# Kernel optimization log

Measured on AMD Instinct MI355X. Metric: run time of the kernel, lower is better.

## Reference

```python
import jax, jax.numpy as jnp
import numpy as np

N = 100000      # num_nodes
E = 1200000     # num_edges (avg degree 12)
F_IN = 64       # num_features
H = 64          # args.hidden_dim
C = 40          # num_classes


def setup_inputs() -> dict:
    key = jax.random.key(0)
    ks = jax.random.split(key, 8)
    x = jax.random.normal(ks[0], (N, F_IN), jnp.float32)
    edge_index = jax.random.randint(ks[1], (2, E), 0, N, dtype=jnp.int64)
    edge_attr = jax.random.uniform(ks[2], (E,), jnp.float32)

    def glorot(k, fi, fo):
        return jax.random.normal(k, (fi, fo), jnp.float32) * jnp.sqrt(2.0 / (fi + fo))

    return {
        "x": x, "edge_index": edge_index, "edge_attr": edge_attr,
        "W1": glorot(ks[3], F_IN, H), "b1": jnp.zeros((H,), jnp.float32),
        "W2": glorot(ks[4], H, H),    "b2": jnp.zeros((H,), jnp.float32),
        "W3": glorot(ks[5], H, H),    "b3": jnp.zeros((H,), jnp.float32),
        "W4": glorot(ks[6], H, C),    "b4": jnp.zeros((C,), jnp.float32),
    }


def _gcn_layer(h, W, b, src, dst, norm):
    # GCNConv: linear transform, gather source features, weight by symmetric
    # norm, scatter-add at targets, add bias.
    h = h @ W                                   # [N, out]
    msg = h[src] * norm[:, None]                # [E+N, out]
    out = jax.ops.segment_sum(msg, dst, num_segments=N)
    return out + b


def reference(x, edge_index, edge_attr, W1, b1, W2, b2, W3, b3, W4, b4):
    # Add self-loops with weight 1 (PyG GCNConv default fill_value=1.)
    loop = jnp.arange(N, dtype=edge_index.dtype)
    src = jnp.concatenate([edge_index[0], loop])
    dst = jnp.concatenate([edge_index[1], loop])
    w = jnp.concatenate([edge_attr, jnp.ones((N,), edge_attr.dtype)])
    # Symmetric normalization: deg^{-1/2}[src] * w * deg^{-1/2}[dst]
    deg = jax.ops.segment_sum(w, dst, num_segments=N)
    dis = jnp.where(deg > 0, jax.lax.rsqrt(jnp.maximum(deg, 1e-12)), 0.0)
    norm = dis[src] * w * dis[dst]

    h = jax.nn.elu(_gcn_layer(x, W1, b1, src, dst, norm))
    h = jax.nn.elu(_gcn_layer(h, W2, b2, src, dst, norm))
    h = jax.nn.elu(_gcn_layer(h, W3, b3, src, dst, norm))
    h = _gcn_layer(h, W4, b4, src, dst, norm)
    return jax.nn.log_softmax(h, axis=1)
```

## Files before the change

### kernel.cpp

```cpp
#include <hip/hip_runtime.h>
#include <hip/hip_fp16.h>
#include <cstdint>
#include <cmath>


#define NPB_SHIFT 9
#define NPB 512
#define CHUNK 4096

__device__ __forceinline__ float fdot2f(__half2 a, __half2 b, float c) {
#if defined(__has_builtin)
#if __has_builtin(__builtin_amdgcn_fdot2)
    typedef _Float16 h2v __attribute__((ext_vector_type(2)));
    return __builtin_amdgcn_fdot2(__builtin_bit_cast(h2v, a),
                                  __builtin_bit_cast(h2v, b), c, false);
#else
    float2 fa = __half22float2(a), fb = __half22float2(b);
    return fmaf(fa.x, fb.x, fmaf(fa.y, fb.y, c));
#endif
#else
    float2 fa = __half22float2(a), fb = __half22float2(b);
    return fmaf(fa.x, fb.x, fmaf(fa.y, fb.y, c));
#endif
}

__device__ __forceinline__ void wave_lds_fence() {
    asm volatile("s_waitcnt lgkmcnt(0)" ::: "memory");
    __builtin_amdgcn_wave_barrier();
    __builtin_amdgcn_sched_barrier(0);
}


__global__ __launch_bounds__(256) void bucket_init_kernel(int* __restrict__ bucket_cnt,
                                                          int nbuck) {
    if ((int)threadIdx.x < nbuck) bucket_cnt[threadIdx.x] = 0;
}

__global__ __launch_bounds__(256) void bucket_count_kernel(const int* __restrict__ dst,
                                                           int* __restrict__ bucket_cnt,
                                                           int* __restrict__ blockbase,
                                                           int nbuck, int E) {
    __shared__ int hist[256];
    int tid = threadIdx.x;
    hist[tid] = 0;
    __syncthreads();
    int base = blockIdx.x * CHUNK;
    #pragma unroll
    for (int u = 0; u < CHUNK / 256; ++u) {
        int e = base + u * 256 + tid;
        if (e < E) atomicAdd(&hist[dst[e] >> NPB_SHIFT], 1);
    }
    __syncthreads();
    if (tid < nbuck)
        blockbase[blockIdx.x * nbuck + tid] = atomicAdd(&bucket_cnt[tid], hist[tid]);
}

__global__ __launch_bounds__(64) void bucket_scan_kernel(const int* __restrict__ bucket_cnt,
                                                         int* __restrict__ bucket_base,
                                                         int nbuck, int E) {
    int lane = threadIdx.x;
    int run = 0;
    for (int b0 = 0; b0 < nbuck; b0 += 64) {
        int i = b0 + lane;
        int v = (i < nbuck) ? bucket_cnt[i] : 0;
        int x = v;
        #pragma unroll
        for (int off = 1; off < 64; off <<= 1) {
            int t = __shfl_up(x, off);
            if (lane >= off) x += t;
        }
        if (i < nbuck) bucket_base[i] = run + x - v;
        run += __shfl(x, 63);
    }
    if (lane == 0) bucket_base[nbuck] = E;
}

__global__ __launch_bounds__(256) void bucket_scatter_kernel(const int* __restrict__ src,
                                                             const int* __restrict__ dst,
                                                             const float* __restrict__ w,
                                                             const int* __restrict__ bucket_base,
                                                             const int* __restrict__ blockbase,
                                                             int2* __restrict__ temp,
                                                             int nbuck, int E) {
    __shared__ int cursor[256];
    int tid = threadIdx.x;
    if (tid < nbuck)
        cursor[tid] = bucket_base[tid] + blockbase[blockIdx.x * nbuck + tid];
    __syncthreads();
    int base = blockIdx.x * CHUNK;
    #pragma unroll
    for (int u = 0; u < CHUNK / 256; ++u) {
        int e = base + u * 256 + tid;
        if (e < E) {
            int d = dst[e];
            int pos = atomicAdd(&cursor[d >> NPB_SHIFT], 1);
            temp[pos] = make_int2(src[e] | ((d & (NPB - 1)) << 17),
                                  __float_as_int(w[e]));
        }
    }
}

__global__ __launch_bounds__(256) void bucket_csr_kernel(const int2* __restrict__ temp,
                                                         const int* __restrict__ bucket_base,
                                                         int* __restrict__ offsets,
                                                         int2* __restrict__ pairs,
                                                         int n, int E) {
    __shared__ int cnt[NPB];
    __shared__ int wtot[4];
    int tid = threadIdx.x;
    int bk = blockIdx.x;
    int base = bucket_base[bk], end = bucket_base[bk + 1];
    cnt[tid] = 0; cnt[tid + 256] = 0;
    __syncthreads();
    for (int j = base + tid; j < end; j += 256)
        atomicAdd(&cnt[temp[j].x >> 17], 1);
    __syncthreads();
    int a0 = cnt[2 * tid], a1 = cnt[2 * tid + 1];
    int s = a0 + a1;
    int lane = tid & 63, wid = tid >> 6;
    int x = s;
    #pragma unroll
    for (int off = 1; off < 64; off <<= 1) {
        int t2 = __shfl_up(x, off);
        if (lane >= off) x += t2;
    }
    if (lane == 63) wtot[wid] = x;
    __syncthreads();
    int wbase = 0;
    #pragma unroll
    for (int wv = 0; wv < 4; ++wv) if (wv < wid) wbase += wtot[wv];
    int e0 = wbase + x - s;
    int abs0 = base + e0, abs1 = base + e0 + a0;
    int node0 = bk * NPB + 2 * tid;
    if (node0 < n)     offsets[node0]     = abs0;
    if (node0 + 1 < n) offsets[node0 + 1] = abs1;
    __syncthreads();
    cnt[2 * tid] = abs0; cnt[2 * tid + 1] = abs1;
    __syncthreads();
    for (int j = base + tid; j < end; j += 256) {
        int2 t2 = temp[j];
        int pos = atomicAdd(&cnt[t2.x >> 17], 1);
        pairs[pos] = make_int2(t2.x & 0x1FFFF, t2.y);
    }
    if (bk == 0 && tid == 0) offsets[n] = E;
}

__global__ __launch_bounds__(256) void rowsum_scale_kernel(const int* __restrict__ offsets,
                                                           const int2* __restrict__ pairs,
                                                           const float* __restrict__ x,
                                                           float* __restrict__ dis,
                                                           __half* __restrict__ g, int n) {
    int node = blockIdx.x * 16 + (threadIdx.x >> 4);
    int q = threadIdx.x & 15;
    if (node >= n) return;
    int j0 = offsets[node], end = offsets[node + 1];
    float s = 0.f;
    for (int j = j0 + q; j < end; j += 16) s += __int_as_float(pairs[j].y);
    #pragma unroll
    for (int off = 8; off; off >>= 1) s += __shfl_xor(s, off);
    float dn = rsqrtf(1.0f + s);
    if (q == 0) dis[node] = dn;
    float4 v = reinterpret_cast<const float4*>(x)[(size_t)node * 16 + q];
    __half2 pk[2];
    pk[0] = __float22half2_rn(make_float2(dn * v.x, dn * v.y));
    pk[1] = __float22half2_rn(make_float2(dn * v.z, dn * v.w));
    reinterpret_cast<float2*>(g + (size_t)node * 64)[q] = *reinterpret_cast<float2*>(pk);
}

__device__ __forceinline__ void accum8(float* acc, float4 rv, float w) {
    const __half2* h = reinterpret_cast<const __half2*>(&rv);
    #pragma unroll
    for (int k = 0; k < 4; ++k) {
        float2 f = __half22float2(h[k]);
        acc[2 * k]     = fmaf(w, f.x, acc[2 * k]);
        acc[2 * k + 1] = fmaf(w, f.y, acc[2 * k + 1]);
    }
}

__device__ __forceinline__ void agg_node(const float4* __restrict__ gt,
                                         const int2* __restrict__ pairs,
                                         int j, int end, int node, int q,
                                         float* __restrict__ acc) {
    for (; j + 4 <= end; j += 4) {
        int2 p0 = pairs[j], p1 = pairs[j + 1], p2 = pairs[j + 2], p3 = pairs[j + 3];
        float4 r0 = gt[(size_t)p0.x * 8 + q];
        float4 r1 = gt[(size_t)p1.x * 8 + q];
        float4 r2 = gt[(size_t)p2.x * 8 + q];
        float4 r3 = gt[(size_t)p3.x * 8 + q];
        accum8(acc, r0, __int_as_float(p0.y));
        accum8(acc, r1, __int_as_float(p1.y));
        accum8(acc, r2, __int_as_float(p2.y));
        accum8(acc, r3, __int_as_float(p3.y));
    }
    for (; j < end; ++j) {
        int2 p = pairs[j];
        float4 r = gt[(size_t)p.x * 8 + q];
        accum8(acc, r, __int_as_float(p.y));
    }
    float4 rs = gt[(size_t)node * 8 + q];
    accum8(acc, rs, 1.0f);
}

__device__ __forceinline__ void phase1_agg(const __half* __restrict__ gin,
                                           const float* __restrict__ dis,
                                           const int* __restrict__ offsets,
                                           const int2* __restrict__ pairs,
                                           __half2 (*rows)[33], int n, int tid,
                                           int blockbase_node) {
    int ln = tid >> 3;
    int q  = tid & 7;
    int gnode = blockbase_node + ln;
    if (gnode < n) {
        const float4* gt = reinterpret_cast<const float4*>(gin);
        float acc[8] = {0.f, 0.f, 0.f, 0.f, 0.f, 0.f, 0.f, 0.f};
        agg_node(gt, pairs, offsets[gnode], offsets[gnode + 1], gnode, q, acc);
        float dn = dis[gnode];
        #pragma unroll
        for (int k2 = 0; k2 < 4; ++k2)
            rows[ln][q * 4 + k2] =
                __float22half2_rn(make_float2(dn * acc[2 * k2], dn * acc[2 * k2 + 1]));
    }
}

__global__ __launch_bounds__(256) void layer_fused_kernel(const __half* __restrict__ gin,
                                                          const float* __restrict__ dis,
                                                          const int* __restrict__ offsets,
                                                          const int2* __restrict__ pairs,
                                                          const float* __restrict__ W,
                                                          const float* __restrict__ b,
                                                          __half* __restrict__ gout, int n) {
    __shared__ __half2 rows[32][33];
    __shared__ __half2 WT[64][33];
    __shared__ float bias_s[64];
    for (int idx = threadIdx.x; idx < 64 * 32; idx += 256) {
        int k2 = idx >> 6, c = idx & 63;
        WT[c][k2] = __float22half2_rn(make_float2(W[(2 * k2) * 64 + c],
                                                  W[(2 * k2 + 1) * 64 + c]));
    }
    if (threadIdx.x < 64) bias_s[threadIdx.x] = b[threadIdx.x];
    __syncthreads();

    int tid = threadIdx.x;
    phase1_agg(gin, dis, offsets, pairs, rows, n, tid, blockIdx.x * 32);
    wave_lds_fence();

    int lane  = tid & 63, wave = tid >> 6;
    int node2 = wave * 8 + (lane & 7);
    int slice = lane >> 3;
    int gnode2 = blockIdx.x * 32 + node2;
    if (gnode2 < n) {
        __half2 h2[32];
        #pragma unroll
        for (int i = 0; i < 32; ++i) h2[i] = rows[node2][i];
        float dn = dis[gnode2];
        int c0 = slice * 8;
        float r[8];
        #pragma unroll
        for (int cc = 0; cc < 8; ++cc) {
            const __half2* wt = &WT[c0 + cc][0];
            float a0 = 0.f, a1 = 0.f, a2 = 0.f, a3 = 0.f;
            #pragma unroll
            for (int i = 0; i < 8; ++i) {
                a0 = fdot2f(h2[4 * i],     wt[4 * i],     a0);
                a1 = fdot2f(h2[4 * i + 1], wt[4 * i + 1], a1);
                a2 = fdot2f(h2[4 * i + 2], wt[4 * i + 2], a2);
                a3 = fdot2f(h2[4 * i + 3], wt[4 * i + 3], a3);
            }
            float v = (a0 + a1) + (a2 + a3) + bias_s[c0 + cc];
            v = (v > 0.f) ? v : expm1f(v);
            r[cc] = dn * v;
        }
        __half2 pk[4];
        pk[0] = __float22half2_rn(make_float2(r[0], r[1]));
        pk[1] = __float22half2_rn(make_float2(r[2], r[3]));
        pk[2] = __float22half2_rn(make_float2(r[4], r[5]));
        pk[3] = __float22half2_rn(make_float2(r[6], r[7]));
        *reinterpret_cast<float4*>(gout + (size_t)gnode2 * 64 + c0) =
            *reinterpret_cast<float4*>(pk);
    }
}

__global__ __launch_bounds__(256) void layer4_fused_kernel(const __half* __restrict__ gin,
                                                           const float* __restrict__ dis,
                                                           const int* __restrict__ offsets,
                                                           const int2* __restrict__ pairs,
                                                           const float* __restrict__ W,
                                                           const float* __restrict__ b,
                                                           float* __restrict__ out, int n) {
    __shared__ __half2 rows[32][33];
    __shared__ __half2 WT[40][33];
    __shared__ float bias_s[40];
    for (int idx = threadIdx.x; idx < 40 * 32; idx += 256) {
        int c = idx % 40, k2 = idx / 40;
        WT[c][k2] = __float22half2_rn(make_float2(W[(2 * k2) * 40 + c],
                                                  W[(2 * k2 + 1) * 40 + c]));
    }
    if (threadIdx.x < 40) bias_s[threadIdx.x] = b[threadIdx.x];
    __syncthreads();

    int tid = threadIdx.x;
    phase1_agg(gin, dis, offsets, pairs, rows, n, tid, blockIdx.x * 32);
    wave_lds_fence();

    int lane  = tid & 63, wave = tid >> 6;
    int node2 = wave * 8 + (lane & 7);
    int slice = lane >> 3;
    int gnode2 = blockIdx.x * 32 + node2;

    float r[5];
    float mp = -__builtin_inff();
    if (gnode2 < n) {
        __half2 h2[32];
        #pragma unroll
        for (int i = 0; i < 32; ++i) h2[i] = rows[node2][i];
        int c0 = slice * 5;
        #pragma unroll
        for (int cc = 0; cc < 5; ++cc) {
            const __half2* wt = &WT[c0 + cc][0];
            float a0 = 0.f, a1 = 0.f, a2 = 0.f, a3 = 0.f;
            #pragma unroll
            for (int i = 0; i < 8; ++i) {
                a0 = fdot2f(h2[4 * i],     wt[4 * i],     a0);
                a1 = fdot2f(h2[4 * i + 1], wt[4 * i + 1], a1);
                a2 = fdot2f(h2[4 * i + 2], wt[4 * i + 2], a2);
                a3 = fdot2f(h2[4 * i + 3], wt[4 * i + 3], a3);
            }
            r[cc] = (a0 + a1) + (a2 + a3) + bias_s[c0 + cc];
            mp = fmaxf(mp, r[cc]);
        }
    }
    mp = fmaxf(mp, __shfl_xor(mp, 8));
    mp = fmaxf(mp, __shfl_xor(mp, 16));
    mp = fmaxf(mp, __shfl_xor(mp, 32));
    float sp = 0.f;
    if (gnode2 < n) {
        #pragma unroll
        for (int cc = 0; cc < 5; ++cc) sp += expf(r[cc] - mp);
    }
    sp += __shfl_xor(sp, 8);
    sp += __shfl_xor(sp, 16);
    sp += __shfl_xor(sp, 32);
    if (gnode2 < n) {
        float ls = logf(sp) + mp;
        float* outp = out + (size_t)gnode2 * 40 + slice * 5;
        #pragma unroll
        for (int cc = 0; cc < 5; ++cc) outp[cc] = r[cc] - ls;
    }
}


static inline size_t align_up(size_t x, size_t a) { return (x + a - 1) & ~(a - 1); }

extern "C" void kernel_launch(void* const* d_in, const int* in_sizes, int n_in,
                              void* d_out, int out_size, void* d_ws, size_t ws_size,
                              hipStream_t stream) {
    const float* x  = (const float*)d_in[0];
    const int*   ei = (const int*)d_in[1];
    const float* ea = (const float*)d_in[2];
    const float* W1 = (const float*)d_in[3];
    const float* b1 = (const float*)d_in[4];
    const float* W2 = (const float*)d_in[5];
    const float* b2 = (const float*)d_in[6];
    const float* W3 = (const float*)d_in[7];
    const float* b3 = (const float*)d_in[8];
    const float* W4 = (const float*)d_in[9];
    const float* b4 = (const float*)d_in[10];

    const int N = in_sizes[0] / 64;
    const int E = in_sizes[1] / 2;

    const int* src = ei;
    const int* dst = ei + E;

    const int nbuck   = (N + NPB - 1) >> NPB_SHIFT;
    const int nblk_ac = (E + CHUNK - 1) / CHUNK;

    char* p = (char*)d_ws;
    int*    offsets     = (int*)p;  p += align_up(((size_t)N + 1) * 4, 256);
    int*    bucket_cnt  = (int*)p;  p += align_up(((size_t)nbuck + 1) * 4, 256);
    int*    bucket_base = (int*)p;  p += align_up(((size_t)nbuck + 1) * 4, 256);
    int*    blockbase   = (int*)p;  p += align_up((size_t)nblk_ac * nbuck * 4, 256);
    float*  dis         = (float*)p; p += align_up((size_t)N * 4, 256);
    int2*   pairs       = (int2*)p;  p += align_up(((size_t)E + 8) * 8, 256);
    int2*   temp        = (int2*)p;  p += align_up(((size_t)E + 8) * 8, 256);
    __half* gA          = (__half*)p; p += align_up((size_t)N * 64 * 2, 256);
    __half* gB          = (__half*)p; p += align_up((size_t)N * 64 * 2, 256);
    (void)ws_size;

    const int nb_g16 = (N + 15) / 16;
    const int nb_f   = (N + 31) / 32;

    bucket_init_kernel<<<1, 256, 0, stream>>>(bucket_cnt, nbuck);
    bucket_count_kernel<<<nblk_ac, 256, 0, stream>>>(dst, bucket_cnt, blockbase, nbuck, E);
    bucket_scan_kernel<<<1, 64, 0, stream>>>(bucket_cnt, bucket_base, nbuck, E);
    bucket_scatter_kernel<<<nblk_ac, 256, 0, stream>>>(src, dst, ea, bucket_base,
                                                       blockbase, temp, nbuck, E);
    bucket_csr_kernel<<<nbuck, 256, 0, stream>>>(temp, bucket_base, offsets, pairs, N, E);
    rowsum_scale_kernel<<<nb_g16, 256, 0, stream>>>(offsets, pairs, x, dis, gA, N);

    layer_fused_kernel<<<nb_f, 256, 0, stream>>>(gA, dis, offsets, pairs, W1, b1, gB, N);
    layer_fused_kernel<<<nb_f, 256, 0, stream>>>(gB, dis, offsets, pairs, W2, b2, gA, N);
    layer_fused_kernel<<<nb_f, 256, 0, stream>>>(gA, dis, offsets, pairs, W3, b3, gB, N);

    layer4_fused_kernel<<<nb_f, 256, 0, stream>>>(gB, dis, offsets, pairs, W4, b4,
                                                  (float*)d_out, N);
}
```

Measured before the change: 207.7 us.

## Accumulate aggregation in packed fp16, unroll gathers by eight, remap lane-to-node

Edge weights are stored as half2 in the CSR pairs, and neighbour aggregation accumulates with packed fp16 FMA (__hfma2) instead of unpacking to fp32. This halves the accumulator registers and the per-edge ALU work. The gather loop is unrolled to 8 independent loads to raise memory-level parallelism. The transform phase also remaps lanes so consecutive lanes share a node, which turns the softmax shuffles into short xor distances. The cost is reduced accumulation precision, since fp16 sums over about 13 terms risk rounding error or overflow.

```diff
diff --git a/kernel.cpp b/kernel.cpp
--- a/kernel.cpp
+++ b/kernel.cpp
@@ -140,7 +140,8 @@
     for (int j = base + tid; j < end; j += 256) {
         int2 t2 = temp[j];
         int pos = atomicAdd(&cnt[t2.x >> 17], 1);
-        pairs[pos] = make_int2(t2.x & 0x1FFFF, t2.y);
+        __half2 w2 = __float2half2_rn(__int_as_float(t2.y));
+        pairs[pos] = make_int2(t2.x & 0x1FFFF, *reinterpret_cast<int*>(&w2));
     }
     if (bk == 0 && tid == 0) offsets[n] = E;
 }
@@ -155,7 +156,10 @@
     if (node >= n) return;
     int j0 = offsets[node], end = offsets[node + 1];
     float s = 0.f;
-    for (int j = j0 + q; j < end; j += 16) s += __int_as_float(pairs[j].y);
+    for (int j = j0 + q; j < end; j += 16) {
+        int wb = pairs[j].y;
+        s += __low2float(*reinterpret_cast<__half2*>(&wb));
+    }
     #pragma unroll
     for (int off = 8; off; off >>= 1) s += __shfl_xor(s, off);
     float dn = rsqrtf(1.0f + s);
@@ -167,38 +171,46 @@
     reinterpret_cast<float2*>(g + (size_t)node * 64)[q] = *reinterpret_cast<float2*>(pk);
 }
 
-__device__ __forceinline__ void accum8(float* acc, float4 rv, float w) {
+__device__ __forceinline__ void accum_pk(__half2* acc, float4 rv, int wbits) {
+    __half2 w2 = *reinterpret_cast<__half2*>(&wbits);
     const __half2* h = reinterpret_cast<const __half2*>(&rv);
-    #pragma unroll
-    for (int k = 0; k < 4; ++k) {
-        float2 f = __half22float2(h[k]);
-        acc[2 * k]     = fmaf(w, f.x, acc[2 * k]);
-        acc[2 * k + 1] = fmaf(w, f.y, acc[2 * k + 1]);
-    }
+    acc[0] = __hfma2(w2, h[0], acc[0]);
+    acc[1] = __hfma2(w2, h[1], acc[1]);
+    acc[2] = __hfma2(w2, h[2], acc[2]);
+    acc[3] = __hfma2(w2, h[3], acc[3]);
 }
 
 __device__ __forceinline__ void agg_node(const float4* __restrict__ gt,
                                          const int2* __restrict__ pairs,
                                          int j, int end, int node, int q,
-                                         float* __restrict__ acc) {
-    for (; j + 4 <= end; j += 4) {
-        int2 p0 = pairs[j], p1 = pairs[j + 1], p2 = pairs[j + 2], p3 = pairs[j + 3];
+                                         __half2* __restrict__ acc) {
+    for (; j + 8 <= end; j += 8) {
+        int2 p[8];
+        #pragma unroll
+        for (int u = 0; u < 8; ++u) p[u] = pairs[j + u];
+        float4 r[8];
+        #pragma unroll
+        for (int u = 0; u < 8; ++u) r[u] = gt[(size_t)p[u].x * 8 + q];
+        #pragma unroll
+        for (int u = 0; u < 8; ++u) accum_pk(acc, r[u], p[u].y);
+    }
+    for (; j + 2 <= end; j += 2) {
+        int2 p0 = pairs[j], p1 = pairs[j + 1];
         float4 r0 = gt[(size_t)p0.x * 8 + q];
         float4 r1 = gt[(size_t)p1.x * 8 + q];
-        float4 r2 = gt[(size_t)p2.x * 8 + q];
-        float4 r3 = gt[(size_t)p3.x * 8 + q];
-        accum8(acc, r0, __int_as_float(p0.y));
-        accum8(acc, r1, __int_as_float(p1.y));
-        accum8(acc, r2, __int_as_float(p2.y));
-        accum8(acc, r3, __int_as_float(p3.y));
-    }
-    for (; j < end; ++j) {
+        accum_pk(acc, r0, p0.y);
+        accum_pk(acc, r1, p1.y);
+    }
+    if (j < end) {
         int2 p = pairs[j];
-        float4 r = gt[(size_t)p.x * 8 + q];
-        accum8(acc, r, __int_as_float(p.y));
+        accum_pk(acc, gt[(size_t)p.x * 8 + q], p.y);
     }
     float4 rs = gt[(size_t)node * 8 + q];
-    accum8(acc, rs, 1.0f);
+    const __half2* h = reinterpret_cast<const __half2*>(&rs);
+    acc[0] = __hadd2(acc[0], h[0]);
+    acc[1] = __hadd2(acc[1], h[1]);
+    acc[2] = __hadd2(acc[2], h[2]);
+    acc[3] = __hadd2(acc[3], h[3]);
 }
 
 __device__ __forceinline__ void phase1_agg(const __half* __restrict__ gin,
@@ -212,13 +224,15 @@
     int gnode = blockbase_node + ln;
     if (gnode < n) {
         const float4* gt = reinterpret_cast<const float4*>(gin);
-        float acc[8] = {0.f, 0.f, 0.f, 0.f, 0.f, 0.f, 0.f, 0.f};
+        __half2 acc[4];
+        acc[0] = acc[1] = acc[2] = acc[3] = __float2half2_rn(0.f);
         agg_node(gt, pairs, offsets[gnode], offsets[gnode + 1], gnode, q, acc);
         float dn = dis[gnode];
         #pragma unroll
-        for (int k2 = 0; k2 < 4; ++k2)
-            rows[ln][q * 4 + k2] =
-                __float22half2_rn(make_float2(dn * acc[2 * k2], dn * acc[2 * k2 + 1]));
+        for (int k2 = 0; k2 < 4; ++k2) {
+            float2 f = __half22float2(acc[k2]);
+            rows[ln][q * 4 + k2] = __float22half2_rn(make_float2(dn * f.x, dn * f.y));
+        }
     }
 }
 
@@ -245,8 +259,8 @@
     wave_lds_fence();
 
     int lane  = tid & 63, wave = tid >> 6;
-    int node2 = wave * 8 + (lane & 7);
-    int slice = lane >> 3;
+    int node2 = wave * 8 + (lane >> 3);
+    int slice = lane & 7;
     int gnode2 = blockIdx.x * 32 + node2;
     if (gnode2 < n) {
         __half2 h2[32];
@@ -303,8 +317,8 @@
     wave_lds_fence();
 
     int lane  = tid & 63, wave = tid >> 6;
-    int node2 = wave * 8 + (lane & 7);
-    int slice = lane >> 3;
+    int node2 = wave * 8 + (lane >> 3);
+    int slice = lane & 7;
     int gnode2 = blockIdx.x * 32 + node2;
 
     float r[5];
@@ -329,17 +343,17 @@
             mp = fmaxf(mp, r[cc]);
         }
     }
-    mp = fmaxf(mp, __shfl_xor(mp, 8));
-    mp = fmaxf(mp, __shfl_xor(mp, 16));
-    mp = fmaxf(mp, __shfl_xor(mp, 32));
+    mp = fmaxf(mp, __shfl_xor(mp, 1));
+    mp = fmaxf(mp, __shfl_xor(mp, 2));
+    mp = fmaxf(mp, __shfl_xor(mp, 4));
     float sp = 0.f;
     if (gnode2 < n) {
         #pragma unroll
         for (int cc = 0; cc < 5; ++cc) sp += expf(r[cc] - mp);
     }
-    sp += __shfl_xor(sp, 8);
-    sp += __shfl_xor(sp, 16);
-    sp += __shfl_xor(sp, 32);
+    sp += __shfl_xor(sp, 1);
+    sp += __shfl_xor(sp, 2);
+    sp += __shfl_xor(sp, 4);
     if (gnode2 < n) {
         float ls = logf(sp) + mp;
         float* outp = out + (size_t)gnode2 * 40 + slice * 5;
```

Result: slower. 218.2 us (+5.1%).

## Process two nodes per thread group in fused layers with interleaved gathers

Applied to the files above, without the earlier changes.

The fused GCN layer kernel now handles 64 nodes per block, and each 8-thread group aggregates two nodes with an interleaved loop that issues four independent row gathers at a time. The aim is more memory-level parallelism per thread and half as many blocks, each loading the transposed weights once. The transform phase runs two passes over the LDS rows. The bucket counter init kernel is also replaced by hipMemsetAsync. The risks are extra register pressure and imbalance when the two nodes have very different degrees.

```diff
diff --git a/kernel.cpp b/kernel.cpp
--- a/kernel.cpp
+++ b/kernel.cpp
@@ -31,11 +31,6 @@
 }
 
 
-__global__ __launch_bounds__(256) void bucket_init_kernel(int* __restrict__ bucket_cnt,
-                                                          int nbuck) {
-    if ((int)threadIdx.x < nbuck) bucket_cnt[threadIdx.x] = 0;
-}
-
 __global__ __launch_bounds__(256) void bucket_count_kernel(const int* __restrict__ dst,
                                                            int* __restrict__ bucket_cnt,
                                                            int* __restrict__ blockbase,
@@ -177,9 +172,9 @@
     }
 }
 
-__device__ __forceinline__ void agg_node(const float4* __restrict__ gt,
+__device__ __forceinline__ void agg_tail(const float4* __restrict__ gt,
                                          const int2* __restrict__ pairs,
-                                         int j, int end, int node, int q,
+                                         int j, int end, int q,
                                          float* __restrict__ acc) {
     for (; j + 4 <= end; j += 4) {
         int2 p0 = pairs[j], p1 = pairs[j + 1], p2 = pairs[j + 2], p3 = pairs[j + 3];
@@ -197,8 +192,121 @@
         float4 r = gt[(size_t)p.x * 8 + q];
         accum8(acc, r, __int_as_float(p.y));
     }
-    float4 rs = gt[(size_t)node * 8 + q];
-    accum8(acc, rs, 1.0f);
+}
+
+__device__ __forceinline__ void phase1_agg_dual(const __half* __restrict__ gin,
+                                                const float* __restrict__ dis,
+                                                const int* __restrict__ offsets,
+                                                const int2* __restrict__ pairs,
+                                                __half2 (*rows)[33], int n, int tid,
+                                                int base_node) {
+    int g = tid >> 3;
+    int q = tid & 7;
+    int nA = base_node + g;
+    int nB = base_node + 32 + g;
+    const float4* gt = reinterpret_cast<const float4*>(gin);
+
+    float accA[8] = {0.f, 0.f, 0.f, 0.f, 0.f, 0.f, 0.f, 0.f};
+    float accB[8] = {0.f, 0.f, 0.f, 0.f, 0.f, 0.f, 0.f, 0.f};
+    int jA = 0, eA = 0, jB = 0, eB = 0;
+    if (nA < n) { jA = offsets[nA]; eA = offsets[nA + 1]; }
+    if (nB < n) { jB = offsets[nB]; eB = offsets[nB + 1]; }
+
+    while (jA + 2 <= eA && jB + 2 <= eB) {
+        int2 a0 = pairs[jA], a1 = pairs[jA + 1];
+        int2 b0 = pairs[jB], b1 = pairs[jB + 1];
+        float4 rA0 = gt[(size_t)a0.x * 8 + q];
+        float4 rA1 = gt[(size_t)a1.x * 8 + q];
+        float4 rB0 = gt[(size_t)b0.x * 8 + q];
+        float4 rB1 = gt[(size_t)b1.x * 8 + q];
+        accum8(accA, rA0, __int_as_float(a0.y));
+        accum8(accA, rA1, __int_as_float(a1.y));
+        accum8(accB, rB0, __int_as_float(b0.y));
+        accum8(accB, rB1, __int_as_float(b1.y));
+        jA += 2; jB += 2;
+    }
+    agg_tail(gt, pairs, jA, eA, q, accA);
+    agg_tail(gt, pairs, jB, eB, q, accB);
+
+    if (nA < n) {
+        float4 rs = gt[(size_t)nA * 8 + q];
+        accum8(accA, rs, 1.0f);
+        float dn = dis[nA];
+        #pragma unroll
+        for (int k2 = 0; k2 < 4; ++k2)
+            rows[g][q * 4 + k2] =
+                __float22half2_rn(make_float2(dn * accA[2 * k2], dn * accA[2 * k2 + 1]));
+    }
+    if (nB < n) {
+        float4 rs = gt[(size_t)nB * 8 + q];
+        accum8(accB, rs, 1.0f);
+        float dn = dis[nB];
+        #pragma unroll
+        for (int k2 = 0; k2 < 4; ++k2)
+            rows[32 + g][q * 4 + k2] =
+                __float22half2_rn(make_float2(dn * accB[2 * k2], dn * accB[2 * k2 + 1]));
+    }
+}
+
+__global__ __launch_bounds__(256) void layer_fused_kernel(const __half* __restrict__ gin,
+                                                          const float* __restrict__ dis,
+                                                          const int* __restrict__ offsets,
+                                                          const int2* __restrict__ pairs,
+                                                          const float* __restrict__ W,
+                                                          const float* __restrict__ b,
+                                                          __half* __restrict__ gout, int n) {
+    __shared__ __half2 rows[64][33];
+    __shared__ __half2 WT[64][33];
+    __shared__ float bias_s[64];
+    for (int idx = threadIdx.x; idx < 64 * 32; idx += 256) {
+        int k2 = idx >> 6, c = idx & 63;
+        WT[c][k2] = __float22half2_rn(make_float2(W[(2 * k2) * 64 + c],
+                                                  W[(2 * k2 + 1) * 64 + c]));
+    }
+    if (threadIdx.x < 64) bias_s[threadIdx.x] = b[threadIdx.x];
+    __syncthreads();
+
+    int tid = threadIdx.x;
+    phase1_agg_dual(gin, dis, offsets, pairs, rows, n, tid, blockIdx.x * 64);
+    wave_lds_fence();
+
+    int lane  = tid & 63, wave = tid >> 6;
+    int slice = lane >> 3;
+    #pragma unroll
+    for (int pass = 0; pass < 2; ++pass) {
+        int node2  = pass * 32 + wave * 8 + (lane & 7);
+        int gnode2 = blockIdx.x * 64 + node2;
+        if (gnode2 < n) {
+            __half2 h2[32];
+            #pragma unroll
+            for (int i = 0; i < 32; ++i) h2[i] = rows[node2][i];
+            float dn = dis[gnode2];
+            int c0 = slice * 8;
+            float r[8];
+            #pragma unroll
+            for (int cc = 0; cc < 8; ++cc) {
+                const __half2* wt = &WT[c0 + cc][0];
+                float a0 = 0.f, a1 = 0.f, a2 = 0.f, a3 = 0.f;
+                #pragma unroll
+                for (int i = 0; i < 8; ++i) {
+                    a0 = fdot2f(h2[4 * i],     wt[4 * i],     a0);
+                    a1 = fdot2f(h2[4 * i + 1], wt[4 * i + 1], a1);
+                    a2 = fdot2f(h2[4 * i + 2], wt[4 * i + 2], a2);
+                    a3 = fdot2f(h2[4 * i + 3], wt[4 * i + 3], a3);
+                }
+                float v = (a0 + a1) + (a2 + a3) + bias_s[c0 + cc];
+                v = (v > 0.f) ? v : expm1f(v);
+                r[cc] = dn * v;
+            }
+            __half2 pk[4];
+            pk[0] = __float22half2_rn(make_float2(r[0], r[1]));
+            pk[1] = __float22half2_rn(make_float2(r[2], r[3]));
+            pk[2] = __float22half2_rn(make_float2(r[4], r[5]));
+            pk[3] = __float22half2_rn(make_float2(r[6], r[7]));
+            *reinterpret_cast<float4*>(gout + (size_t)gnode2 * 64 + c0) =
+                *reinterpret_cast<float4*>(pk);
+        }
+    }
 }
 
 __device__ __forceinline__ void phase1_agg(const __half* __restrict__ gin,
@@ -213,70 +321,14 @@
     if (gnode < n) {
         const float4* gt = reinterpret_cast<const float4*>(gin);
         float acc[8] = {0.f, 0.f, 0.f, 0.f, 0.f, 0.f, 0.f, 0.f};
-        agg_node(gt, pairs, offsets[gnode], offsets[gnode + 1], gnode, q, acc);
+        agg_tail(gt, pairs, offsets[gnode], offsets[gnode + 1], q, acc);
+        float4 rs = gt[(size_t)gnode * 8 + q];
+        accum8(acc, rs, 1.0f);
         float dn = dis[gnode];
         #pragma unroll
         for (int k2 = 0; k2 < 4; ++k2)
             rows[ln][q * 4 + k2] =
                 __float22half2_rn(make_float2(dn * acc[2 * k2], dn * acc[2 * k2 + 1]));
-    }
-}
-
-__global__ __launch_bounds__(256) void layer_fused_kernel(const __half* __restrict__ gin,
-                                                          const float* __restrict__ dis,
-                                                          const int* __restrict__ offsets,
-                                                          const int2* __restrict__ pairs,
-                                                          const float* __restrict__ W,
-                                                          const float* __restrict__ b,
-                                                          __half* __restrict__ gout, int n) {
-    __shared__ __half2 rows[32][33];
-    __shared__ __half2 WT[64][33];
-    __shared__ float bias_s[64];
-    for (int idx = threadIdx.x; idx < 64 * 32; idx += 256) {
-        int k2 = idx >> 6, c = idx & 63;
-        WT[c][k2] = __float22half2_rn(make_float2(W[(2 * k2) * 64 + c],
-                                                  W[(2 * k2 + 1) * 64 + c]));
-    }
-    if (threadIdx.x < 64) bias_s[threadIdx.x] = b[threadIdx.x];
-    __syncthreads();
-
-    int tid = threadIdx.x;
-    phase1_agg(gin, dis, offsets, pairs, rows, n, tid, blockIdx.x * 32);
-    wave_lds_fence();
-
-    int lane  = tid & 63, wave = tid >> 6;
-    int node2 = wave * 8 + (lane & 7);
-    int slice = lane >> 3;
-    int gnode2 = blockIdx.x * 32 + node2;
-    if (gnode2 < n) {
-        __half2 h2[32];
-        #pragma unroll
-        for (int i = 0; i < 32; ++i) h2[i] = rows[node2][i];
-        float dn = dis[gnode2];
-        int c0 = slice * 8;
-        float r[8];
-        #pragma unroll
-        for (int cc = 0; cc < 8; ++cc) {
-            const __half2* wt = &WT[c0 + cc][0];
-            float a0 = 0.f, a1 = 0.f, a2 = 0.f, a3 = 0.f;
-            #pragma unroll
-            for (int i = 0; i < 8; ++i) {
-                a0 = fdot2f(h2[4 * i],     wt[4 * i],     a0);
-                a1 = fdot2f(h2[4 * i + 1], wt[4 * i + 1], a1);
-                a2 = fdot2f(h2[4 * i + 2], wt[4 * i + 2], a2);
-                a3 = fdot2f(h2[4 * i + 3], wt[4 * i + 3], a3);
-            }
-            float v = (a0 + a1) + (a2 + a3) + bias_s[c0 + cc];
-            v = (v > 0.f) ? v : expm1f(v);
-            r[cc] = dn * v;
-        }
-        __half2 pk[4];
-        pk[0] = __float22half2_rn(make_float2(r[0], r[1]));
-        pk[1] = __float22half2_rn(make_float2(r[2], r[3]));
-        pk[2] = __float22half2_rn(make_float2(r[4], r[5]));
-        pk[3] = __float22half2_rn(make_float2(r[6], r[7]));
-        *reinterpret_cast<float4*>(gout + (size_t)gnode2 * 64 + c0) =
-            *reinterpret_cast<float4*>(pk);
     }
 }
 
@@ -388,9 +440,10 @@
     (void)ws_size;
 
     const int nb_g16 = (N + 15) / 16;
-    const int nb_f   = (N + 31) / 32;
-
-    bucket_init_kernel<<<1, 256, 0, stream>>>(bucket_cnt, nbuck);
+    const int nb_f   = (N + 63) / 64;
+    const int nb_f4  = (N + 31) / 32;
+
+    hipMemsetAsync(bucket_cnt, 0, (size_t)(nbuck + 1) * 4, stream);
     bucket_count_kernel<<<nblk_ac, 256, 0, stream>>>(dst, bucket_cnt, blockbase, nbuck, E);
     bucket_scan_kernel<<<1, 64, 0, stream>>>(bucket_cnt, bucket_base, nbuck, E);
     bucket_scatter_kernel<<<nblk_ac, 256, 0, stream>>>(src, dst, ea, bucket_base,
@@ -402,6 +455,6 @@
     layer_fused_kernel<<<nb_f, 256, 0, stream>>>(gB, dis, offsets, pairs, W2, b2, gA, N);
     layer_fused_kernel<<<nb_f, 256, 0, stream>>>(gA, dis, offsets, pairs, W3, b3, gB, N);
 
-    layer4_fused_kernel<<<nb_f, 256, 0, stream>>>(gB, dis, offsets, pairs, W4, b4,
-                                                  (float*)d_out, N);
-}
+    layer4_fused_kernel<<<nb_f4, 256, 0, stream>>>(gB, dis, offsets, pairs, W4, b4,
+                                                   (float*)d_out, N);
+}
```

After: 257.9 us. 1.24x slower.
